# Kernel optimization log

Measured on AMD Instinct MI355X. Metric: run time of the kernel, lower is better.

## Reference

```python
import jax, jax.numpy as jnp
import numpy as np

G = 16       # groups
GRID = 25    # hardcoded self.grid
EPS = 1e-5   # BatchNorm eps


def _gconv(x, w, pad):
    # x: (B, Cin, H, W), w: (Cout, Cin//G, kh, kw); grouped conv, stride 1
    return jax.lax.conv_general_dilated(
        x, w, window_strides=(1, 1), padding=[(pad, pad), (pad, pad)],
        feature_group_count=G)


def _bn_relu(h, g, b, m, v):
    # h: (G, B, C, H, W); per-group-instance BN params: (G, C). Inference BN.
    scale = (g / jnp.sqrt(v + EPS))[:, None, :, None, None]
    return jax.nn.relu((h - m[:, None, :, None, None]) * scale + b[:, None, :, None, None])


def setup_inputs() -> dict:
    key = jax.random.key(0)
    ks = jax.random.split(key, 11)
    B, C, H, W = 2, 256, 24, 24
    AC = GRID * C  # 6400 affinity channels
    return {
        "x":  jax.random.normal(ks[0], (B, C, H, W), jnp.float32),
        "W1": jax.random.normal(ks[1], (G, C, C // G, 3, 3), jnp.float32) * 0.05,
        "g1": jax.random.uniform(ks[2], (G, C), jnp.float32, 0.5, 1.5),
        "b1": jax.random.normal(ks[3], (G, C), jnp.float32) * 0.1,
        "m1": jax.random.normal(ks[4], (G, C), jnp.float32) * 0.1,
        "v1": jax.random.uniform(ks[5], (G, C), jnp.float32, 0.5, 1.5),
        "W2": jax.random.normal(ks[6], (G, AC, C // G, 1, 1), jnp.float32) * 0.05,
        "g2": jax.random.uniform(ks[7], (G, AC), jnp.float32, 0.5, 1.5),
        "b2": jax.random.normal(ks[8], (G, AC), jnp.float32) * 0.1,
        "m2": jax.random.normal(ks[9], (G, AC), jnp.float32) * 0.1,
        "v2": jax.random.uniform(ks[10], (G, AC), jnp.float32, 0.5, 1.5),
    }


def reference(x, W1, g1, b1, m1, v1, W2, g2, b2, m2, v2):
    B, C, H, W = x.shape
    Cg = C // G
    # 16 independent grouped 3x3 convs over the same input, batched via vmap
    h1 = jax.vmap(lambda w: _gconv(x, w, 1))(W1)          # (G, B, C, H, W)
    h1 = _bn_relu(h1, g1, b1, m1, v1)
    # grouped 1x1 conv with padding=1 (faithful to source -> spatial grows to H+2, W+2)
    a = jax.vmap(lambda h, w: _gconv(h, w, 1))(h1, W2)    # (G, B, 25C, H+2, W+2)
    a = _bn_relu(a, g2, b2, m2, v2)
    pooled = a.mean(axis=(-2, -1))                        # adaptive avg pool -> (G, B, 25C)
    xv = pooled.reshape(G, B, G, GRID * Cg)               # (G, B, G, 25*Cg)
    aff = jnp.einsum('ibkm,iblm->ibkl', xv, xv)           # (G, B, G, G) = theta @ phi
    idx = jnp.arange(G)
    aff_i = aff[idx, :, idx, :] / G                       # aff[:, i], /N  -> (G, B, G)
    ex = h1.reshape(G, B, G, Cg * H * W)
    # torch.matmul((B,G), (B,G,M)) broadcasts 2-D lhs -> (B, B, M); kept faithfully
    z = jnp.einsum('ipk,iqkm->ipqm', aff_i, ex)           # (G, B, B, Cg*H*W)
    z = z.reshape(G, B, B, Cg, H, W).transpose(1, 0, 2, 3, 4, 5)
    return z.reshape(B, G * B * Cg, H, W)                 # (B, B*C, H, W)
```

## Files before the change

kernel.cpp:

```cpp
#include <hip/hip_runtime.h>
#include <hip/hip_bf16.h>


typedef __attribute__((ext_vector_type(8))) short short8;
typedef __attribute__((ext_vector_type(4))) float f32x4;

static __device__ __forceinline__ unsigned short f2bf(float x) {
    unsigned u = __float_as_uint(x);
    unsigned r = (u + 0x7fffu + ((u >> 16) & 1u)) >> 16;
    return (unsigned short)r;
}

#define WA_OFF   33696
#define WLB_OFF  23040
#define B2_OFF   35840
#define PACC_OFF 37440
#define ZP_OFF   40096
#define S1_OFF   40112
#define BB1_OFF  40176
#define SMEM_BYTES 40240

__global__ __launch_bounds__(256) void k12_fused(
    const float* __restrict__ xin,
    const float* __restrict__ W1,
    const float* __restrict__ g1, const float* __restrict__ b1,
    const float* __restrict__ m1, const float* __restrict__ v1,
    const float* __restrict__ W2,
    const float* __restrict__ g2, const float* __restrict__ b2,
    const float* __restrict__ m2, const float* __restrict__ v2,
    unsigned short* __restrict__ h1b,
    float* __restrict__ pooled)
{
    __shared__ __align__(16) char smem[SMEM_BYTES];
    short* xs    = (short*)smem;
    short* wAp   = (short*)(smem + WA_OFF);
    short* hsb   = (short*)smem;
    short* wlb   = (short*)(smem + WLB_OFF);
    float* bias2 = (float*)(smem + B2_OFF);
    float* pacc  = (float*)(smem + PACC_OFF);
    float* scale1 = (float*)(smem + S1_OFF);
    float* bias1  = (float*)(smem + BB1_OFF);

    int bid = blockIdx.x;
    int i = bid >> 5, b = (bid >> 4) & 1, g = bid & 15;
    int t = threadIdx.x;

    int* xz = (int*)xs;
    for (int idx = t; idx < 27*26*12; idx += 256) xz[idx] = 0;
    if (t < 4) ((int*)(smem + ZP_OFF))[t] = 0;
    if (t < 16) {
        int c = i*256 + g*16 + t;
        float sc = g1[c] * rsqrtf(v1[c] + 1e-5f);
        scale1[t] = sc;
        bias1[t]  = b1[c] - m1[c] * sc;
    }
    __syncthreads();

    const float* xb = &xin[(b*256 + g*16)*576];
    for (int idx = t; idx < 9216; idx += 256) {
        int ci = idx / 576; int s = idx - ci*576;
        int y = s / 24; int x = s - y*24;
        xs[((y+1)*26 + (x+1))*24 + ci] = (short)f2bf(xb[idx]);
    }
    const float* wb = &W1[(i*256 + g*16)*144];
    for (int idx = t; idx < 2560; idx += 256) {
        int kk = idx >> 9, rem = idx & 511, co = rem >> 5, k = rem & 31;
        int tap = 2*kk + (k >> 4), ci = k & 15;
        float val = (tap < 9) ? wb[co*144 + ci*9 + tap] * scale1[co] : 0.f;
        wAp[(kk*16 + co)*40 + k] = (short)f2bf(val);
    }
    __syncthreads();

    int l = t & 63, w = t >> 6;
    int quad = l >> 4, rc = l & 15;

    f32x4 dreg[9];
    {
        int ci0 = (quad & 1) * 8;
        short8 afr[5];
#pragma unroll
        for (int kk = 0; kk < 5; kk++)
            afr[kk] = *(const short8*)&wAp[(kk*16 + rc)*40 + quad*8];
        f32x4 cb1 = *(const f32x4*)&bias1[quad*4];

        const int offE[5] = {0, 48, 648, 1248, 1296};
        const int offO[5] = {24, 624, 672, 1272, 1872};
        int off[5];
#pragma unroll
        for (int kk = 0; kk < 5; kk++) off[kk] = (quad >= 2) ? offO[kk] : offE[kk];

#pragma unroll
        for (int tt = 0; tt < 9; tt++) {
            int s = (w*9 + tt)*16 + rc;
            int y = s / 24; int x = s - y*24;
            int base = (y*26 + x)*24 + ci0;
            f32x4 acc = cb1;
#pragma unroll
            for (int kk = 0; kk < 5; kk++) {
                short8 bf = *(const short8*)&xs[base + off[kk]];
                acc = __builtin_amdgcn_mfma_f32_16x16x32_bf16(afr[kk], bf, acc, 0, 0, 0);
            }
#pragma unroll
            for (int r = 0; r < 4; r++) acc[r] = fmaxf(acc[r], 0.f);
            dreg[tt] = acc;
        }
    }
    __syncthreads();

    {
        unsigned short* hout = &h1b[((i*2 + b)*256 + g*16)*576];
#pragma unroll
        for (int tt = 0; tt < 9; tt++) {
            int s = (w*9 + tt)*16 + rc;
            f32x4 acc = dreg[tt];
            unsigned short e0 = f2bf(acc[0]), e1 = f2bf(acc[1]);
            unsigned short e2 = f2bf(acc[2]), e3 = f2bf(acc[3]);
            unsigned p0 = (unsigned)e0 | ((unsigned)e1 << 16);
            unsigned p1 = (unsigned)e2 | ((unsigned)e3 << 16);
            uint2 pk = {p0, p1};
            *(uint2*)&hsb[s*20 + quad*4] = pk;
            hout[(quad*4 + 0)*576 + s] = e0;
            hout[(quad*4 + 1)*576 + s] = e1;
            hout[(quad*4 + 2)*576 + s] = e2;
            hout[(quad*4 + 3)*576 + s] = e3;
        }
    }

    for (int m = t; m < 400; m += 256) {
        pacc[m] = 0.f;
        int o = i*6400 + g*400 + m;
        float s2 = g2[o] * rsqrtf(v2[o] + 1e-5f);
        bias2[m] = b2[o] - m2[o] * s2;
        const float4* wr = (const float4*)&W2[o*16];
#pragma unroll
        for (int q = 0; q < 4; q++) {
            float4 wv = wr[q];
            wlb[m*16 + q*4 + 0] = (short)f2bf(wv.x * s2);
            wlb[m*16 + q*4 + 1] = (short)f2bf(wv.y * s2);
            wlb[m*16 + q*4 + 2] = (short)f2bf(wv.z * s2);
            wlb[m*16 + q*4 + 3] = (short)f2bf(wv.w * s2);
        }
    }
    __syncthreads();

    {
        int q8 = (quad & 1) * 8;
        short8 af2[9];
#pragma unroll
        for (int u = 0; u < 9; u++) {
            int boff = (l < 32) ? ((((w*9 + u)*16 + rc)*20 + q8)*2) : ZP_OFF;
            af2[u] = *(const short8*)(smem + boff);
        }
        for (int mt = 0; mt < 25; mt++) {
            int m0 = mt*16;
            int woff = (l < 32) ? (WLB_OFF + ((m0 + rc)*16 + q8)*2) : ZP_OFF;
            short8 wf = *(const short8*)(smem + woff);
            float be = bias2[m0 + rc];
            f32x4 cb = {be, be, be, be};

            f32x4 accv = {0.f, 0.f, 0.f, 0.f};
#pragma unroll
            for (int u = 0; u < 9; u++) {
                f32x4 d = __builtin_amdgcn_mfma_f32_16x16x32_bf16(af2[u], wf, cb, 0, 0, 0);
#pragma unroll
                for (int r = 0; r < 4; r++)
                    accv[r] += fmaxf(d[r], 0.f);
            }
            float a = (accv[0] + accv[1]) + (accv[2] + accv[3]);
            a += __shfl_xor(a, 16);
            a += __shfl_xor(a, 32);
            if (l < 16)
                atomicAdd(&pacc[m0 + l], a);
        }
    }
    __syncthreads();

    const float inv = 1.f / 676.f;
    for (int m = t; m < 400; m += 256) {
        float be = bias2[m];
        pooled[(i*2+b)*6400 + g*400 + m] =
            (pacc[m] + 100.f * fmaxf(be, 0.f)) * inv;
    }
}

__global__ __launch_bounds__(256) void k34_out(const float* __restrict__ pooled,
                                               const unsigned short* __restrict__ h1b,
                                               float* __restrict__ out)
{
    __shared__ float parts[256];
    __shared__ float av[2][16];
    int bid = blockIdx.x;
    int i = bid >> 5, q = (bid >> 4) & 1, cg = bid & 15;
    int t = threadIdx.x;

    {
        int pl = t >> 3;
        int u  = t & 7;
        int p = pl >> 4, lidx = pl & 15;
        const float* pb = &pooled[(i*2 + p)*6400];
        const float* pt = &pb[i*400];
        const float* pl2 = &pb[lidx*400];
        float s = 0.f;
        for (int m = u*50; m < u*50 + 50; m++) s = fmaf(pt[m], pl2[m], s);
        parts[t] = s;
    }
    __syncthreads();
    if (t < 32) {
        float s = 0.f;
#pragma unroll
        for (int u = 0; u < 8; u++) s += parts[t*8 + u];
        av[t >> 4][t & 15] = s * (1.f/16.f);
    }
    __syncthreads();

    const unsigned short* hb = &h1b[((i*2 + q)*256 + cg)*576];
    int ch = i*32 + q*16 + cg;
    for (int s = t; s < 576; s += 256) {
        float acc0 = 0.f, acc1 = 0.f;
#pragma unroll
        for (int k = 0; k < 16; k++) {
            float v = __uint_as_float((unsigned)hb[k*9216 + s] << 16);
            acc0 = fmaf(av[0][k], v, acc0);
            acc1 = fmaf(av[1][k], v, acc1);
        }
        out[ch*576 + s]         = acc0;
        out[(512 + ch)*576 + s] = acc1;
    }
}

extern "C" void kernel_launch(void* const* d_in, const int* in_sizes, int n_in,
                              void* d_out, int out_size, void* d_ws, size_t ws_size,
                              hipStream_t stream)
{
    const float* x  = (const float*)d_in[0];
    const float* W1 = (const float*)d_in[1];
    const float* g1 = (const float*)d_in[2];
    const float* b1 = (const float*)d_in[3];
    const float* m1 = (const float*)d_in[4];
    const float* v1 = (const float*)d_in[5];
    const float* W2 = (const float*)d_in[6];
    const float* g2 = (const float*)d_in[7];
    const float* b2 = (const float*)d_in[8];
    const float* m2 = (const float*)d_in[9];
    const float* v2 = (const float*)d_in[10];

    unsigned short* h1b = (unsigned short*)d_ws;
    float* pooled = (float*)(h1b + 16*2*256*576);

    float* out = (float*)d_out;

    hipLaunchKernelGGL(k12_fused, dim3(512), dim3(256), 0, stream,
                       x, W1, g1, b1, m1, v1, W2, g2, b2, m2, v2, h1b, pooled);
    hipLaunchKernelGGL(k34_out,   dim3(512), dim3(256), 0, stream,
                       pooled, h1b, out);
}
```

Before: 119.0 us.

## Split fused conv kernel into two half-image blocks with global atomic pooling

Each (i,b,g) block is split into two blocks, one per half of the image (12 rows plus halo), using 192 threads each, which doubles the grid to 1024 blocks. The blocks no longer share an LDS accumulator. Each half-block adds its pool contributions with atomics into its own global partial buffer, which is zeroed by a memset, and the consumer kernel sums the two halves. The aim is more parallelism, since 512 blocks underfill the GPU, and a smaller LDS footprint to raise occupancy. The cost is an extra memset launch, duplicated W2 weight preparation in both half-blocks, and global atomics.

```diff
diff --git a/kernel.cpp b/kernel.cpp
--- a/kernel.cpp
+++ b/kernel.cpp
@@ -11,16 +11,16 @@
     return (unsigned short)r;
 }
 
-#define WA_OFF   33696
-#define WLB_OFF  23040
-#define B2_OFF   35840
-#define PACC_OFF 37440
-#define ZP_OFF   40096
-#define S1_OFF   40112
-#define BB1_OFF  40176
-#define SMEM_BYTES 40240
-
-__global__ __launch_bounds__(256) void k12_fused(
+#define XS_OFF   0
+#define WA_OFF   11648
+#define HS_OFF   16768
+#define WLB_OFF  25984
+#define B2_OFF   38784
+#define BB1_OFF  40384
+#define ZP_OFF   0
+#define SMEM_BYTES 40448
+
+__global__ __launch_bounds__(192, 3) void k12_fused(
     const float* __restrict__ xin,
     const float* __restrict__ W1,
     const float* __restrict__ g1, const float* __restrict__ b1,
@@ -29,105 +29,61 @@
     const float* __restrict__ g2, const float* __restrict__ b2,
     const float* __restrict__ m2, const float* __restrict__ v2,
     unsigned short* __restrict__ h1b,
-    float* __restrict__ pooled)
+    float* __restrict__ ph)
 {
     __shared__ __align__(16) char smem[SMEM_BYTES];
     short* xs    = (short*)smem;
     short* wAp   = (short*)(smem + WA_OFF);
-    short* hsb   = (short*)smem;
+    short* hsb   = (short*)(smem + HS_OFF);
     short* wlb   = (short*)(smem + WLB_OFF);
     float* bias2 = (float*)(smem + B2_OFF);
-    float* pacc  = (float*)(smem + PACC_OFF);
-    float* scale1 = (float*)(smem + S1_OFF);
-    float* bias1  = (float*)(smem + BB1_OFF);
-
-    int bid = blockIdx.x;
-    int i = bid >> 5, b = (bid >> 4) & 1, g = bid & 15;
+    float* bias1 = (float*)(smem + BB1_OFF);
+
+    int bid  = blockIdx.x;
+    int hsel = bid >> 9;
+    int core = bid & 511;
+    int i = core >> 5, b = (core >> 4) & 1, g = core & 15;
     int t = threadIdx.x;
-
-    int* xz = (int*)xs;
-    for (int idx = t; idx < 27*26*12; idx += 256) xz[idx] = 0;
-    if (t < 4) ((int*)(smem + ZP_OFF))[t] = 0;
+    int r0 = hsel * 12;
+
+    {
+        int zrow = hsel ? 13 : 0;
+        int* xz = (int*)xs;
+        for (int idx = t; idx < 432; idx += 192) {
+            int c = idx >> 3, j = idx & 7;
+            int lr, col;
+            if (c < 26) { lr = zrow; col = c; }
+            else        { int cc = c - 26; lr = cc >> 1; col = (cc & 1) ? 25 : 0; }
+            xz[(lr*26 + col)*8 + j] = 0;
+        }
+    }
     if (t < 16) {
         int c = i*256 + g*16 + t;
         float sc = g1[c] * rsqrtf(v1[c] + 1e-5f);
-        scale1[t] = sc;
-        bias1[t]  = b1[c] - m1[c] * sc;
-    }
-    __syncthreads();
-
-    const float* xb = &xin[(b*256 + g*16)*576];
-    for (int idx = t; idx < 9216; idx += 256) {
-        int ci = idx / 576; int s = idx - ci*576;
-        int y = s / 24; int x = s - y*24;
-        xs[((y+1)*26 + (x+1))*24 + ci] = (short)f2bf(xb[idx]);
-    }
-    const float* wb = &W1[(i*256 + g*16)*144];
-    for (int idx = t; idx < 2560; idx += 256) {
-        int kk = idx >> 9, rem = idx & 511, co = rem >> 5, k = rem & 31;
-        int tap = 2*kk + (k >> 4), ci = k & 15;
-        float val = (tap < 9) ? wb[co*144 + ci*9 + tap] * scale1[co] : 0.f;
-        wAp[(kk*16 + co)*40 + k] = (short)f2bf(val);
-    }
-    __syncthreads();
-
-    int l = t & 63, w = t >> 6;
-    int quad = l >> 4, rc = l & 15;
-
-    f32x4 dreg[9];
-    {
-        int ci0 = (quad & 1) * 8;
-        short8 afr[5];
-#pragma unroll
-        for (int kk = 0; kk < 5; kk++)
-            afr[kk] = *(const short8*)&wAp[(kk*16 + rc)*40 + quad*8];
-        f32x4 cb1 = *(const f32x4*)&bias1[quad*4];
-
-        const int offE[5] = {0, 48, 648, 1248, 1296};
-        const int offO[5] = {24, 624, 672, 1272, 1872};
-        int off[5];
-#pragma unroll
-        for (int kk = 0; kk < 5; kk++) off[kk] = (quad >= 2) ? offO[kk] : offE[kk];
-
-#pragma unroll
-        for (int tt = 0; tt < 9; tt++) {
-            int s = (w*9 + tt)*16 + rc;
-            int y = s / 24; int x = s - y*24;
-            int base = (y*26 + x)*24 + ci0;
-            f32x4 acc = cb1;
-#pragma unroll
-            for (int kk = 0; kk < 5; kk++) {
-                short8 bf = *(const short8*)&xs[base + off[kk]];
-                acc = __builtin_amdgcn_mfma_f32_16x16x32_bf16(afr[kk], bf, acc, 0, 0, 0);
-            }
-#pragma unroll
-            for (int r = 0; r < 4; r++) acc[r] = fmaxf(acc[r], 0.f);
-            dreg[tt] = acc;
-        }
-    }
-    __syncthreads();
-
-    {
-        unsigned short* hout = &h1b[((i*2 + b)*256 + g*16)*576];
-#pragma unroll
-        for (int tt = 0; tt < 9; tt++) {
-            int s = (w*9 + tt)*16 + rc;
-            f32x4 acc = dreg[tt];
-            unsigned short e0 = f2bf(acc[0]), e1 = f2bf(acc[1]);
-            unsigned short e2 = f2bf(acc[2]), e3 = f2bf(acc[3]);
-            unsigned p0 = (unsigned)e0 | ((unsigned)e1 << 16);
-            unsigned p1 = (unsigned)e2 | ((unsigned)e3 << 16);
-            uint2 pk = {p0, p1};
-            *(uint2*)&hsb[s*20 + quad*4] = pk;
-            hout[(quad*4 + 0)*576 + s] = e0;
-            hout[(quad*4 + 1)*576 + s] = e1;
-            hout[(quad*4 + 2)*576 + s] = e2;
-            hout[(quad*4 + 3)*576 + s] = e3;
-        }
-    }
-
-    for (int m = t; m < 400; m += 256) {
-        pacc[m] = 0.f;
+        bias1[t] = b1[c] - m1[c] * sc;
+    }
+    {
+        const float* xb = &xin[(b*256 + g*16)*576];
+        for (int idx = t; idx < 5376; idx += 192) {
+            int ci = idx / 336; int rem = idx - ci*336;
+            int lr = rem / 24;  int x = rem - lr*24;
+            int r = r0 + lr - 1;
+            if ((unsigned)r < 24u)
+                xs[(lr*26 + x + 1)*16 + ci] = (short)f2bf(xb[ci*576 + r*24 + x]);
+        }
+    }
+    {
+        const float* wb = &W1[(i*256 + g*16)*144];
+        for (int idx = t; idx < 2560; idx += 192) {
+            int kk = idx >> 9, rem = idx & 511, co = rem >> 5, k = rem & 31;
+            int tap = 2*kk + (k >> 4), ci = k & 15;
+            int c = i*256 + g*16 + co;
+            float sc = g1[c] * rsqrtf(v1[c] + 1e-5f);
+            float val = (tap < 9) ? wb[co*144 + ci*9 + tap] * sc : 0.f;
+            wAp[(kk*16 + co)*32 + k] = (short)f2bf(val);
+        }
+    }
+    for (int m = t; m < 400; m += 192) {
         int o = i*6400 + g*400 + m;
         float s2 = g2[o] * rsqrtf(v2[o] + 1e-5f);
         bias2[m] = b2[o] - m2[o] * s2;
@@ -143,24 +99,80 @@
     }
     __syncthreads();
 
-    {
-        int q8 = (quad & 1) * 8;
-        short8 af2[9];
-#pragma unroll
-        for (int u = 0; u < 9; u++) {
-            int boff = (l < 32) ? ((((w*9 + u)*16 + rc)*20 + q8)*2) : ZP_OFF;
+    int l = t & 63, w = t >> 6;
+    int quad = l >> 4, rc = l & 15;
+
+    f32x4 dreg[6];
+    {
+        int ci0 = (quad & 1) * 8;
+        short8 afr[5];
+#pragma unroll
+        for (int kk = 0; kk < 5; kk++)
+            afr[kk] = *(const short8*)&wAp[(kk*16 + rc)*32 + quad*8];
+        f32x4 cb1 = *(const f32x4*)&bias1[quad*4];
+
+        const int offE[5] = {0, 32, 432, 832, 864};
+        const int offO[5] = {16, 416, 448, 848, 848};
+        int off[5];
+#pragma unroll
+        for (int kk = 0; kk < 5; kk++) off[kk] = (quad >= 2) ? offO[kk] : offE[kk];
+
+#pragma unroll
+        for (int tt = 0; tt < 6; tt++) {
+            int sl = (w*6 + tt)*16 + rc;
+            int ly = sl / 24; int x = sl - ly*24;
+            int base = (ly*26 + x)*16 + ci0;
+            f32x4 acc = cb1;
+#pragma unroll
+            for (int kk = 0; kk < 5; kk++) {
+                short8 bf = *(const short8*)&xs[base + off[kk]];
+                acc = __builtin_amdgcn_mfma_f32_16x16x32_bf16(afr[kk], bf, acc, 0, 0, 0);
+            }
+#pragma unroll
+            for (int r = 0; r < 4; r++) acc[r] = fmaxf(acc[r], 0.f);
+            dreg[tt] = acc;
+        }
+    }
+
+    {
+        unsigned short* hout = &h1b[((i*2 + b)*256 + g*16)*576 + hsel*288];
+#pragma unroll
+        for (int tt = 0; tt < 6; tt++) {
+            int sl = (w*6 + tt)*16 + rc;
+            f32x4 acc = dreg[tt];
+            unsigned short e0 = f2bf(acc[0]), e1 = f2bf(acc[1]);
+            unsigned short e2 = f2bf(acc[2]), e3 = f2bf(acc[3]);
+            uint2 pk = {(unsigned)e0 | ((unsigned)e1 << 16),
+                        (unsigned)e2 | ((unsigned)e3 << 16)};
+            *(uint2*)&hsb[sl*16 + quad*4] = pk;
+            hout[(quad*4 + 0)*576 + sl] = e0;
+            hout[(quad*4 + 1)*576 + sl] = e1;
+            hout[(quad*4 + 2)*576 + sl] = e2;
+            hout[(quad*4 + 3)*576 + sl] = e3;
+        }
+    }
+
+    {
+        int qb = (quad & 1) * 16;
+        short8 af2[6];
+#pragma unroll
+        for (int u = 0; u < 6; u++) {
+            int boff = (l < 32) ? (HS_OFF + ((w*6 + u)*16 + rc)*32 + qb) : ZP_OFF;
             af2[u] = *(const short8*)(smem + boff);
         }
+        const float inv = 1.f / 676.f;
+        float* pout = &ph[hsel*204800 + (i*2 + b)*6400 + g*400];
+        bool bmaster = (hsel == 0) && (w == 0);
         for (int mt = 0; mt < 25; mt++) {
             int m0 = mt*16;
-            int woff = (l < 32) ? (WLB_OFF + ((m0 + rc)*16 + q8)*2) : ZP_OFF;
+            int woff = (l < 32) ? (WLB_OFF + (m0 + rc)*32 + qb) : ZP_OFF;
             short8 wf = *(const short8*)(smem + woff);
             float be = bias2[m0 + rc];
             f32x4 cb = {be, be, be, be};
 
             f32x4 accv = {0.f, 0.f, 0.f, 0.f};
 #pragma unroll
-            for (int u = 0; u < 9; u++) {
+            for (int u = 0; u < 6; u++) {
                 f32x4 d = __builtin_amdgcn_mfma_f32_16x16x32_bf16(af2[u], wf, cb, 0, 0, 0);
 #pragma unroll
                 for (int r = 0; r < 4; r++)
@@ -169,21 +181,14 @@
             float a = (accv[0] + accv[1]) + (accv[2] + accv[3]);
             a += __shfl_xor(a, 16);
             a += __shfl_xor(a, 32);
+            if (bmaster) a += 100.f * fmaxf(be, 0.f);
             if (l < 16)
-                atomicAdd(&pacc[m0 + l], a);
-        }
-    }
-    __syncthreads();
-
-    const float inv = 1.f / 676.f;
-    for (int m = t; m < 400; m += 256) {
-        float be = bias2[m];
-        pooled[(i*2+b)*6400 + g*400 + m] =
-            (pacc[m] + 100.f * fmaxf(be, 0.f)) * inv;
-    }
-}
-
-__global__ __launch_bounds__(256) void k34_out(const float* __restrict__ pooled,
+                atomicAdd(&pout[m0 + l], a * inv);
+        }
+    }
+}
+
+__global__ __launch_bounds__(256) void k34_out(const float* __restrict__ ph,
                                                const unsigned short* __restrict__ h1b,
                                                float* __restrict__ out)
 {
@@ -197,11 +202,13 @@
         int pl = t >> 3;
         int u  = t & 7;
         int p = pl >> 4, lidx = pl & 15;
-        const float* pb = &pooled[(i*2 + p)*6400];
-        const float* pt = &pb[i*400];
-        const float* pl2 = &pb[lidx*400];
+        const float* pb0 = &ph[(i*2 + p)*6400];
+        const float* pb1 = pb0 + 204800;
+        const float* t0 = &pb0[i*400];    const float* t1 = &pb1[i*400];
+        const float* l0 = &pb0[lidx*400]; const float* l1 = &pb1[lidx*400];
         float s = 0.f;
-        for (int m = u*50; m < u*50 + 50; m++) s = fmaf(pt[m], pl2[m], s);
+        for (int m = u*50; m < u*50 + 50; m++)
+            s = fmaf(t0[m] + t1[m], l0[m] + l1[m], s);
         parts[t] = s;
     }
     __syncthreads();
@@ -245,12 +252,14 @@
     const float* v2 = (const float*)d_in[10];
 
     unsigned short* h1b = (unsigned short*)d_ws;
-    float* pooled = (float*)(h1b + 16*2*256*576);
+    float* ph = (float*)(h1b + 16*2*256*576);
 
     float* out = (float*)d_out;
 
-    hipLaunchKernelGGL(k12_fused, dim3(512), dim3(256), 0, stream,
-                       x, W1, g1, b1, m1, v1, W2, g2, b2, m2, v2, h1b, pooled);
-    hipLaunchKernelGGL(k34_out,   dim3(512), dim3(256), 0, stream,
-                       pooled, h1b, out);
-}
+    hipMemsetAsync(ph, 0, 2*204800*sizeof(float), stream);
+
+    hipLaunchKernelGGL(k12_fused, dim3(1024), dim3(192), 0, stream,
+                       x, W1, g1, b1, m1, v1, W2, g2, b2, m2, v2, h1b, ph);
+    hipLaunchKernelGGL(k34_out,   dim3(512),  dim3(256), 0, stream,
+                       ph, h1b, out);
+}
```

Result: slower. 145.0 us (+21.9%).

## Split affinity computation into separate kernel and vectorize output pass

Applied to the files above, without the earlier changes.

Before, each of the 512 output blocks recomputed the same affinity dot products from the pooled features. These are now computed once in a small 32-block kernel that writes them to workspace, and the output kernel only reads them. The output kernel also handles two pixels per thread with 32-bit bf16 loads and float2 stores. The cost is an extra kernel launch and a dependency through global memory.

```diff
diff --git a/kernel.cpp b/kernel.cpp
--- a/kernel.cpp
+++ b/kernel.cpp
@@ -183,48 +183,60 @@
     }
 }
 
-__global__ __launch_bounds__(256) void k34_out(const float* __restrict__ pooled,
-                                               const unsigned short* __restrict__ h1b,
-                                               float* __restrict__ out)
-{
+__global__ __launch_bounds__(256) void k3_aff(const float* __restrict__ pooled,
+                                              float* __restrict__ aff)
+{
+    __shared__ float th[400];
     __shared__ float parts[256];
-    __shared__ float av[2][16];
+    int bid = blockIdx.x;
+    int i = bid >> 1;
+    int t = threadIdx.x;
+    const float* pb = &pooled[bid*6400];
+    for (int idx = t; idx < 400; idx += 256) th[idx] = pb[i*400 + idx];
+    __syncthreads();
+    int l = t >> 4, p = t & 15;
+    float sum = 0.f;
+    const float* pl = &pb[l*400];
+    for (int m = p*25; m < p*25 + 25; m++) sum = fmaf(th[m], pl[m], sum);
+    parts[t] = sum;
+    __syncthreads();
+    if (t < 16) {
+        float s = 0.f;
+        for (int pp = 0; pp < 16; pp++) s += parts[t*16 + pp];
+        aff[bid*16 + t] = s * (1.f/16.f);
+    }
+}
+
+__global__ __launch_bounds__(256) void k4_out(const unsigned short* __restrict__ h1b,
+                                              const float* __restrict__ aff,
+                                              float* __restrict__ out)
+{
+    __shared__ float a0[16], a1[16];
     int bid = blockIdx.x;
     int i = bid >> 5, q = (bid >> 4) & 1, cg = bid & 15;
     int t = threadIdx.x;
-
-    {
-        int pl = t >> 3;
-        int u  = t & 7;
-        int p = pl >> 4, lidx = pl & 15;
-        const float* pb = &pooled[(i*2 + p)*6400];
-        const float* pt = &pb[i*400];
-        const float* pl2 = &pb[lidx*400];
-        float s = 0.f;
-        for (int m = u*50; m < u*50 + 50; m++) s = fmaf(pt[m], pl2[m], s);
-        parts[t] = s;
-    }
-    __syncthreads();
-    if (t < 32) {
-        float s = 0.f;
-#pragma unroll
-        for (int u = 0; u < 8; u++) s += parts[t*8 + u];
-        av[t >> 4][t & 15] = s * (1.f/16.f);
-    }
-    __syncthreads();
-
-    const unsigned short* hb = &h1b[((i*2 + q)*256 + cg)*576];
+    if (t < 16) a0[t] = aff[(i*2+0)*16 + t];
+    else if (t < 32) a1[t-16] = aff[(i*2+1)*16 + (t-16)];
+    __syncthreads();
+    const unsigned short* hb = &h1b[((i*2+q)*256 + cg)*576];
     int ch = i*32 + q*16 + cg;
-    for (int s = t; s < 576; s += 256) {
-        float acc0 = 0.f, acc1 = 0.f;
+    for (int pp = t; pp < 288; pp += 256) {
+        int s = pp*2;
+        float acc0a = 0.f, acc0b = 0.f, acc1a = 0.f, acc1b = 0.f;
 #pragma unroll
         for (int k = 0; k < 16; k++) {
-            float v = __uint_as_float((unsigned)hb[k*9216 + s] << 16);
-            acc0 = fmaf(av[0][k], v, acc0);
-            acc1 = fmaf(av[1][k], v, acc1);
-        }
-        out[ch*576 + s]         = acc0;
-        out[(512 + ch)*576 + s] = acc1;
+            unsigned hv = *(const unsigned*)&hb[k*9216 + s];
+            float va = __uint_as_float(hv << 16);
+            float vb = __uint_as_float(hv & 0xffff0000u);
+            acc0a = fmaf(a0[k], va, acc0a);
+            acc0b = fmaf(a0[k], vb, acc0b);
+            acc1a = fmaf(a1[k], va, acc1a);
+            acc1b = fmaf(a1[k], vb, acc1b);
+        }
+        float2 o0 = {acc0a, acc0b};
+        float2 o1 = {acc1a, acc1b};
+        *(float2*)&out[ch*576 + s]         = o0;
+        *(float2*)&out[(512 + ch)*576 + s] = o1;
     }
 }
 
@@ -246,11 +258,14 @@
 
     unsigned short* h1b = (unsigned short*)d_ws;
     float* pooled = (float*)(h1b + 16*2*256*576);
+    float* aff    = pooled + 204800;
 
     float* out = (float*)d_out;
 
     hipLaunchKernelGGL(k12_fused, dim3(512), dim3(256), 0, stream,
                        x, W1, g1, b1, m1, v1, W2, g2, b2, m2, v2, h1b, pooled);
-    hipLaunchKernelGGL(k34_out,   dim3(512), dim3(256), 0, stream,
-                       pooled, h1b, out);
-}
+    hipLaunchKernelGGL(k3_aff,    dim3(32),  dim3(256), 0, stream,
+                       pooled, aff);
+    hipLaunchKernelGGL(k4_out,    dim3(512), dim3(256), 0, stream,
+                       h1b, aff, out);
+}
```

New measurement: 116.5 us. 2.1% less time.
